# Kernel optimization log

Hardware: AMD Instinct MI355X
Metric: run time of the kernel (lower is better)

Reference implementation:

```python
import jax, jax.numpy as jnp
import numpy as np
from jax import lax

# Static problem sizes (see shape_source)
B, C, N = 32, 512, 64
SENTS_PER_VIDEO = 4
TARGETS_PER_SENT = 2
S = B * SENTS_PER_VIDEO          # 128 sentences
M = S * TARGETS_PER_SENT         # 256 target moments
P = N * (N + 1) // 2             # 2080 valid proposals (upper-tri mask2d)
T_TEMP = 0.1
MARGIN = 0.0
NEG_IOU = 0.5
K_TOP = 1                        # pos_topk
WEIGHT = 1.0


def setup_inputs() -> dict:
    key = jax.random.key(0)
    k1, k2, k3, k4 = jax.random.split(key, 4)
    return {
        "video_feats": jax.random.normal(k1, (B, C, N, N), jnp.float32),
        "sents_feats": jax.random.normal(k2, (S, C), jnp.float32),
        "num_sentences": jnp.full((B,), SENTS_PER_VIDEO, jnp.int32),
        "num_targets": jnp.full((S,), TARGETS_PER_SENT, jnp.int32),
        "iou2d": jax.random.uniform(k3, (S, N, N), jnp.float32),
        "iou2ds": jax.random.uniform(k4, (M, N, N), jnp.float32),
        "mask2d": jnp.triu(jnp.ones((N, N), bool)),
        "epoch": 0,  # < start_DNS_epoch -> DNS branch skipped
    }


def _log_cross_entropy(pos_scores, all_scores, neg_mask, t, m):
    # Faithful to LogCrossEntropy.forward
    pos_exp = jnp.exp((pos_scores - m) / t)
    neg_exp_sum = jnp.sum(jnp.exp(all_scores / t) * neg_mask, axis=-1)
    loss = -((pos_scores - m) / t - jnp.log(pos_exp + neg_exp_sum))
    return jnp.mean(loss)


def _l2_normalize(x, axis=-1, eps=1e-12):
    n = jnp.linalg.norm(x, axis=axis, keepdims=True)
    return x / jnp.maximum(n, eps)


def reference(video_feats, sents_feats, num_sentences, num_targets,
              iou2d, iou2ds, mask2d, epoch):
    # Compact valid proposals (P is static: upper-triangular mask2d)
    idx = jnp.nonzero(mask2d.reshape(-1), size=P)[0]              # (P,)
    v = video_feats.reshape(B, C, N * N)[:, :, idx]               # (B,C,P)
    v = jnp.transpose(v, (0, 2, 1))                               # (B,P,C)
    iou2d_f = iou2d.reshape(S, N * N)[:, idx]                     # (S,P)
    iou2ds_f = iou2ds.reshape(M, N * N)[:, idx]                   # (M,P)

    v = _l2_normalize(v)
    sents = _l2_normalize(sents_feats)

    scatter_s2v = jnp.repeat(jnp.arange(B), num_sentences, total_repeat_length=S)
    scatter_m2s = jnp.repeat(jnp.arange(S), num_targets, total_repeat_length=M)
    scatter_m2v = scatter_s2v[scatter_m2s]

    # top-K proposals per target moment by IoU
    topk_idx = lax.top_k(iou2ds_f, K_TOP)[1]                      # (M,K)
    topk_v = jnp.take_along_axis(v[scatter_m2v], topk_idx[:, :, None], axis=1)  # (M,K,C)

    # inter-video loss
    inter_video_pos = jnp.einsum('mkc,mc->mk', topk_v, sents[scatter_m2s])  # (M,K)
    inter_video_all = jnp.einsum('mkc,sc->mks', topk_v, sents)              # (M,K,S)
    inter_video_neg_mask = (~jnp.eye(S, dtype=bool))[scatter_m2s][:, None, :]  # (M,1,S)
    loss_inter_video = _log_cross_entropy(
        inter_video_pos, inter_video_all, inter_video_neg_mask, T_TEMP, MARGIN)

    # inter-query loss
    inter_query_pos = inter_video_pos                              # (M,K)
    inter_query_all = (sents @ v.reshape(B * P, C).T)[:, None, :]  # (S,1,B*P)
    # pos_mask: block-diagonal per video, refined by IoU > neg_iou inside own block
    onehot = jnp.eye(B, dtype=bool)[scatter_s2v]                   # (S,B)
    pos_mask = (onehot[:, :, None] & (iou2d_f > NEG_IOU)[:, None, :]).reshape(S, B * P)
    inter_query_neg_mask = (~pos_mask)[:, None, :]                 # (S,1,B*P)
    loss_inter_query = _log_cross_entropy(
        inter_query_pos, inter_query_all[scatter_m2s],
        inter_query_neg_mask[scatter_m2s], T_TEMP, MARGIN)

    total = (loss_inter_video + loss_inter_query) * WEIGHT
    return total, loss_inter_video, loss_inter_query
```

## Files before the change

kernel.cpp:

```cpp
#include <hip/hip_runtime.h>
#include <cstdint>

#define BB 32
#define CC 512
#define NSQ 4096
#define SS 128
#define MM 256
#define PP 2080
#define JJ (BB*PP)

#define WS_SN     0
#define WS_SNB    262144
#define WS_IDX    393216
#define WS_IV     401536
#define WS_NEGQ   532608

typedef short bf16x8 __attribute__((ext_vector_type(8)));
typedef float f32x4  __attribute__((ext_vector_type(4)));

__device__ __forceinline__ unsigned short f2bf(float x) {
    unsigned int u = __float_as_uint(x);
    unsigned int r = (u + 0x7fffu + ((u >> 16) & 1u)) >> 16;
    return (unsigned short)r;
}

__global__ void k_prep(const float* __restrict__ sents, float* __restrict__ sn,
                       unsigned short* __restrict__ snb,
                       int* __restrict__ idx, float* __restrict__ negq) {
    const int blk = blockIdx.x, t = threadIdx.x;
    if (blk < 128) {
        __shared__ float red[256];
        const float* row = sents + (size_t)blk * CC;
        float x0 = row[t], x1 = row[t + 256];
        red[t] = x0 * x0 + x1 * x1;
        __syncthreads();
        for (int off = 128; off > 0; off >>= 1) {
            if (t < off) red[t] += red[t + off];
            __syncthreads();
        }
        float rn = 1.0f / fmaxf(sqrtf(red[0]), 1e-12f);
        float y0 = x0 * rn, y1 = x1 * rn;
        sn[(size_t)blk * CC + t]        = y0;
        sn[(size_t)blk * CC + t + 256]  = y1;
        snb[(size_t)blk * CC + t]       = f2bf(y0);
        snb[(size_t)blk * CC + t + 256] = f2bf(y1);
    } else if (blk < 144) {
        int i = (blk - 128) * 256 + t;
        int r = i >> 6, c = i & 63;
        if (c >= r) {
            int p = r * 64 - (r * (r - 1)) / 2 + (c - r);
            idx[p] = i;
        }
    } else {
        if (t < 128) negq[t] = 0.0f;
    }
}

__global__ void k_fused(const float* __restrict__ video, const float* __restrict__ sn,
                        const float* __restrict__ iou2ds, const int* __restrict__ idx,
                        float* __restrict__ iv) {
    const int m = blockIdx.x, t = threadIdx.x;
    __shared__ float sv[256];
    __shared__ int   si[256];
    __shared__ float tvs[512];
    __shared__ float red[256];

    {
        float best = -1e30f; int bi = 1 << 30;
        const float* row = iou2ds + (size_t)m * NSQ;
        for (int p = t; p < PP; p += 256) {
            float v = row[idx[p]];
            if (v > best || (v == best && p < bi)) { best = v; bi = p; }
        }
        sv[t] = best; si[t] = bi;
        __syncthreads();
        for (int off = 128; off > 0; off >>= 1) {
            if (t < off) {
                float v2 = sv[t + off]; int i2 = si[t + off];
                if (v2 > sv[t] || (v2 == sv[t] && i2 < si[t])) { sv[t] = v2; si[t] = i2; }
            }
            __syncthreads();
        }
    }
    const int flat = idx[si[0]];
    const int b = m >> 3;

    const float* base = video + (size_t)b * CC * NSQ + flat;
    float x0 = base[(size_t)t * NSQ];
    float x1 = base[(size_t)(t + 256) * NSQ];
    red[t] = x0 * x0 + x1 * x1;
    __syncthreads();
    for (int off = 128; off > 0; off >>= 1) {
        if (t < off) red[t] += red[t + off];
        __syncthreads();
    }
    float rn = 1.0f / fmaxf(sqrtf(red[0]), 1e-12f);
    tvs[t] = x0 * rn;
    tvs[t + 256] = x1 * rn;
    __syncthreads();

    const int s = t & 127, h = t >> 7;
    const float4* a4 = (const float4*)(tvs + h * 256);
    const float4* b4 = (const float4*)(sn + (size_t)s * CC + h * 256);
    float acc = 0.f;
#pragma unroll 8
    for (int c = 0; c < 64; c++) {
        float4 a = a4[c], bb = b4[c];
        acc += a.x * bb.x + a.y * bb.y + a.z * bb.z + a.w * bb.w;
    }
    __syncthreads();
    red[t] = acc;
    __syncthreads();
    if (t < 128) iv[(size_t)m * SS + t] = red[t] + red[t + 128];
}

#define BK 64
#define LDK 72

__global__ __launch_bounds__(256)
void k_big(const float* __restrict__ video, const unsigned short* __restrict__ snb,
           const float* __restrict__ iou2d, const int* __restrict__ idx,
           float* __restrict__ negq) {
    __shared__ unsigned short sA[128 * LDK];
    __shared__ unsigned short vB[128 * LDK];
    __shared__ int   colb[128], colflat[128];
    __shared__ float colrn[128];
    __shared__ float sqpart[256];
    __shared__ float red[128][17];

    const int t    = threadIdx.x;
    const int w    = t >> 6;
    const int lane = t & 63;
    const int q    = lane >> 4;
    const int l15  = lane & 15;
    const int j0   = blockIdx.x * 128;

    if (t < 128) {
        int col = j0 + t;
        int b = col / PP;
        colb[t] = b;
        colflat[t] = idx[col - b * PP];
    }

    const int jj = t & 127;
    const int kh = t >> 7;
    int colL = j0 + jj;
    int bL = colL / PP;
    int flatL = idx[colL - bL * PP];
    const float* vbase = video + (size_t)bL * (CC * NSQ) + flatL;

    f32x4 acc[2][8];
#pragma unroll
    for (int i = 0; i < 2; i++)
#pragma unroll
        for (int j = 0; j < 8; j++) acc[i][j] = (f32x4){0.f, 0.f, 0.f, 0.f};

    float sqa = 0.f;

    for (int k0 = 0; k0 < CC; k0 += BK) {
        __syncthreads();
#pragma unroll
        for (int it = 0; it < 4; it++) {
            int lin = t + it * 256;
            int row = lin >> 3, kc = (lin & 7) * 8;
            bf16x8 v = *(const bf16x8*)(snb + (size_t)row * CC + k0 + kc);
            *(bf16x8*)(sA + row * LDK + kc) = v;
        }
        {
            const float* vp = vbase + (size_t)(k0 + kh * 32) * NSQ;
#pragma unroll
            for (int g = 0; g < 4; g++) {
                unsigned short buf[8];
#pragma unroll
                for (int i = 0; i < 8; i++) {
                    float x = vp[(size_t)(g * 8 + i) * NSQ];
                    sqa += x * x;
                    buf[i] = f2bf(x);
                }
                *(bf16x8*)(vB + jj * LDK + kh * 32 + g * 8) = *(bf16x8*)buf;
            }
        }
        __syncthreads();
#pragma unroll
        for (int ks = 0; ks < BK; ks += 32) {
            bf16x8 a[2], bfr[8];
#pragma unroll
            for (int rt = 0; rt < 2; rt++) {
                int row = w * 32 + rt * 16 + l15;
                a[rt] = *(const bf16x8*)(sA + row * LDK + ks + q * 8);
            }
#pragma unroll
            for (int ct = 0; ct < 8; ct++) {
                int col = ct * 16 + l15;
                bfr[ct] = *(const bf16x8*)(vB + col * LDK + ks + q * 8);
            }
#pragma unroll
            for (int rt = 0; rt < 2; rt++)
#pragma unroll
                for (int ct = 0; ct < 8; ct++)
                    acc[rt][ct] = __builtin_amdgcn_mfma_f32_16x16x32_bf16(
                        a[rt], bfr[ct], acc[rt][ct], 0, 0, 0);
        }
    }

    sqpart[t] = sqa;
    __syncthreads();
    if (t < 128) colrn[t] = 1.0f / fmaxf(sqrtf(sqpart[t] + sqpart[t + 128]), 1e-12f);
    __syncthreads();

#pragma unroll
    for (int rt = 0; rt < 2; rt++) {
#pragma unroll
        for (int r = 0; r < 4; r++) {
            int s = w * 32 + rt * 16 + q * 4 + r;
            float rowsum = 0.f;
#pragma unroll
            for (int ct = 0; ct < 8; ct++) {
                int c = ct * 16 + l15;
                float sc = acc[rt][ct][r] * colrn[c];
                float e = expf(sc * 10.0f);
                if ((s >> 2) == colb[c]) {
                    if (iou2d[(size_t)s * NSQ + colflat[c]] > 0.5f) e = 0.f;
                }
                rowsum += e;
            }
            red[s][l15] = rowsum;
        }
    }
    __syncthreads();
    if (t < 128) {
        float tot = 0.f;
#pragma unroll
        for (int x = 0; x < 16; x++) tot += red[t][x];
        atomicAdd(&negq[t], tot);
    }
}

__global__ void k_final(const float* __restrict__ iv, const float* __restrict__ negq,
                        float* __restrict__ out) {
    const int t = threadIdx.x;
    __shared__ float rv[256], rq[256];
    const float* row = iv + (size_t)t * SS;
    const int ms = t >> 1;
    float pos = row[ms];
    float nv = 0.f;
    for (int s = 0; s < SS; s++) {
        float e = expf(row[s] * 10.0f);
        if (s == ms) e = 0.f;
        nv += e;
    }
    float pe = expf(pos * 10.0f);
    float lv = logf(pe + nv) - pos * 10.0f;
    float lq = logf(pe + negq[ms]) - pos * 10.0f;
    rv[t] = lv; rq[t] = lq;
    __syncthreads();
    for (int off = 128; off > 0; off >>= 1) {
        if (t < off) { rv[t] += rv[t + off]; rq[t] += rq[t + off]; }
        __syncthreads();
    }
    if (t == 0) {
        float liv = rv[0] / 256.f, liq = rq[0] / 256.f;
        out[0] = liv + liq;
        out[1] = liv;
        out[2] = liq;
    }
}

extern "C" void kernel_launch(void* const* d_in, const int* in_sizes, int n_in,
                              void* d_out, int out_size, void* d_ws, size_t ws_size,
                              hipStream_t stream) {
    const float* video  = (const float*)d_in[0];
    const float* sents  = (const float*)d_in[1];
    const float* iou2d  = (const float*)d_in[4];
    const float* iou2ds = (const float*)d_in[5];
    float* out = (float*)d_out;

    char* ws = (char*)d_ws;
    float*          sn   = (float*)(ws + WS_SN);
    unsigned short* snb  = (unsigned short*)(ws + WS_SNB);
    int*            idx  = (int*)(ws + WS_IDX);
    float*          iv   = (float*)(ws + WS_IV);
    float*          negq = (float*)(ws + WS_NEGQ);

    k_prep <<<145, 256, 0, stream>>>(sents, sn, snb, idx, negq);
    k_big  <<<JJ / 128, 256, 0, stream>>>(video, snb, iou2d, idx, negq);
    k_fused<<<MM,  256, 0, stream>>>(video, sn, iou2ds, idx, iv);
    k_final<<<1,   256, 0, stream>>>(iv, negq, out);
}
```

Measured before the change: 439.0 us.

## Merge big GEMM and topk kernels into one launch with swizzled LDS

Combines k_fused and k_big into a single kernel whose first 256 blocks handle the per-target top-1 path and the remaining blocks run the bf16 MFMA similarity tile. This removes one launch and lets the two independent workloads overlap on the device. It also swaps padded LDS rows for an XOR swizzle to avoid bank conflicts, replaces the shared-memory row reduction with wave shuffles plus more atomics, uses __expf, and sets launch_bounds occupancy 4. The union-based shared memory shrinks the footprint, but register pressure may rise under the occupancy hint.

Measured after the change: 489.6 us. 1.12x slower.

```diff
diff --git a/kernel.cpp b/kernel.cpp
--- a/kernel.cpp
+++ b/kernel.cpp
@@ -8,6 +8,7 @@
 #define MM 256
 #define PP 2080
 #define JJ (BB*PP)
+#define NBIG (JJ/128)
 
 #define WS_SN     0
 #define WS_SNB    262144
@@ -56,90 +57,98 @@
     }
 }
 
-__global__ void k_fused(const float* __restrict__ video, const float* __restrict__ sn,
-                        const float* __restrict__ iou2ds, const int* __restrict__ idx,
-                        float* __restrict__ iv) {
-    const int m = blockIdx.x, t = threadIdx.x;
-    __shared__ float sv[256];
-    __shared__ int   si[256];
-    __shared__ float tvs[512];
-    __shared__ float red[256];
-
-    {
-        float best = -1e30f; int bi = 1 << 30;
-        const float* row = iou2ds + (size_t)m * NSQ;
-        for (int p = t; p < PP; p += 256) {
-            float v = row[idx[p]];
-            if (v > best || (v == best && p < bi)) { best = v; bi = p; }
-        }
-        sv[t] = best; si[t] = bi;
+
+union SMem {
+    struct {
+        unsigned short sA[128 * 64];
+        unsigned short vB[128 * 64];
+        int   colb[128];
+        int   colflat[128];
+        float colrn[128];
+        float sqpart[256];
+    } big;
+    struct {
+        float sv[256];
+        int   si[256];
+        float tvs[512];
+        float red[256];
+    } fus;
+};
+
+__global__ __launch_bounds__(256, 4)
+void k_mega(const float* __restrict__ video, const float* __restrict__ sn,
+            const unsigned short* __restrict__ snb,
+            const float* __restrict__ iou2d, const float* __restrict__ iou2ds,
+            const int* __restrict__ idx,
+            float* __restrict__ iv, float* __restrict__ negq) {
+    __shared__ SMem sm;
+    const int t = threadIdx.x;
+
+    if (blockIdx.x < MM) {
+        const int m = blockIdx.x;
+        {
+            float best = -1e30f; int bi = 1 << 30;
+            const float* row = iou2ds + (size_t)m * NSQ;
+            for (int p = t; p < PP; p += 256) {
+                float v = row[idx[p]];
+                if (v > best || (v == best && p < bi)) { best = v; bi = p; }
+            }
+            sm.fus.sv[t] = best; sm.fus.si[t] = bi;
+            __syncthreads();
+            for (int off = 128; off > 0; off >>= 1) {
+                if (t < off) {
+                    float v2 = sm.fus.sv[t + off]; int i2 = sm.fus.si[t + off];
+                    if (v2 > sm.fus.sv[t] || (v2 == sm.fus.sv[t] && i2 < sm.fus.si[t])) {
+                        sm.fus.sv[t] = v2; sm.fus.si[t] = i2;
+                    }
+                }
+                __syncthreads();
+            }
+        }
+        const int flat = idx[sm.fus.si[0]];
+        const int b = m >> 3;
+
+        const float* base = video + (size_t)b * CC * NSQ + flat;
+        float x0 = base[(size_t)t * NSQ];
+        float x1 = base[(size_t)(t + 256) * NSQ];
+        sm.fus.red[t] = x0 * x0 + x1 * x1;
         __syncthreads();
         for (int off = 128; off > 0; off >>= 1) {
-            if (t < off) {
-                float v2 = sv[t + off]; int i2 = si[t + off];
-                if (v2 > sv[t] || (v2 == sv[t] && i2 < si[t])) { sv[t] = v2; si[t] = i2; }
-            }
+            if (t < off) sm.fus.red[t] += sm.fus.red[t + off];
             __syncthreads();
         }
-    }
-    const int flat = idx[si[0]];
-    const int b = m >> 3;
-
-    const float* base = video + (size_t)b * CC * NSQ + flat;
-    float x0 = base[(size_t)t * NSQ];
-    float x1 = base[(size_t)(t + 256) * NSQ];
-    red[t] = x0 * x0 + x1 * x1;
-    __syncthreads();
-    for (int off = 128; off > 0; off >>= 1) {
-        if (t < off) red[t] += red[t + off];
-        __syncthreads();
-    }
-    float rn = 1.0f / fmaxf(sqrtf(red[0]), 1e-12f);
-    tvs[t] = x0 * rn;
-    tvs[t + 256] = x1 * rn;
-    __syncthreads();
-
-    const int s = t & 127, h = t >> 7;
-    const float4* a4 = (const float4*)(tvs + h * 256);
-    const float4* b4 = (const float4*)(sn + (size_t)s * CC + h * 256);
-    float acc = 0.f;
+        float rn = 1.0f / fmaxf(sqrtf(sm.fus.red[0]), 1e-12f);
+        sm.fus.tvs[t] = x0 * rn;
+        sm.fus.tvs[t + 256] = x1 * rn;
+        __syncthreads();
+
+        const int s = t & 127, h = t >> 7;
+        const float4* a4 = (const float4*)(sm.fus.tvs + h * 256);
+        const float4* b4 = (const float4*)(sn + (size_t)s * CC + h * 256);
+        float acc = 0.f;
 #pragma unroll 8
-    for (int c = 0; c < 64; c++) {
-        float4 a = a4[c], bb = b4[c];
-        acc += a.x * bb.x + a.y * bb.y + a.z * bb.z + a.w * bb.w;
-    }
-    __syncthreads();
-    red[t] = acc;
-    __syncthreads();
-    if (t < 128) iv[(size_t)m * SS + t] = red[t] + red[t + 128];
-}
-
-#define BK 64
-#define LDK 72
-
-__global__ __launch_bounds__(256)
-void k_big(const float* __restrict__ video, const unsigned short* __restrict__ snb,
-           const float* __restrict__ iou2d, const int* __restrict__ idx,
-           float* __restrict__ negq) {
-    __shared__ unsigned short sA[128 * LDK];
-    __shared__ unsigned short vB[128 * LDK];
-    __shared__ int   colb[128], colflat[128];
-    __shared__ float colrn[128];
-    __shared__ float sqpart[256];
-    __shared__ float red[128][17];
-
-    const int t    = threadIdx.x;
+        for (int c = 0; c < 64; c++) {
+            float4 a = a4[c], bb = b4[c];
+            acc += a.x * bb.x + a.y * bb.y + a.z * bb.z + a.w * bb.w;
+        }
+        __syncthreads();
+        sm.fus.red[t] = acc;
+        __syncthreads();
+        if (t < 128) iv[(size_t)m * SS + t] = sm.fus.red[t] + sm.fus.red[t + 128];
+        return;
+    }
+
     const int w    = t >> 6;
     const int lane = t & 63;
     const int q    = lane >> 4;
     const int l15  = lane & 15;
-    const int j0   = blockIdx.x * 128;
+    const int j0   = (blockIdx.x - MM) * 128;
 
     if (t < 128) {
         int col = j0 + t;
         int b = col / PP;
-        colb[t] = b;
-        colflat[t] = idx[col - b * PP];
+        sm.big.colb[t] = b;
+        sm.big.colflat[t] = idx[col - b * PP];
     }
 
     const int jj = t & 127;
@@ -156,15 +165,17 @@
         for (int j = 0; j < 8; j++) acc[i][j] = (f32x4){0.f, 0.f, 0.f, 0.f};
 
     float sqa = 0.f;
-
-    for (int k0 = 0; k0 < CC; k0 += BK) {
+    const int swzA_w = jj & 7;
+    (void)swzA_w;
+
+    for (int k0 = 0; k0 < CC; k0 += 64) {
         __syncthreads();
 #pragma unroll
         for (int it = 0; it < 4; it++) {
             int lin = t + it * 256;
-            int row = lin >> 3, kc = (lin & 7) * 8;
-            bf16x8 v = *(const bf16x8*)(snb + (size_t)row * CC + k0 + kc);
-            *(bf16x8*)(sA + row * LDK + kc) = v;
+            int row = lin >> 3, G = lin & 7;
+            bf16x8 v = *(const bf16x8*)(snb + (size_t)row * CC + k0 + G * 8);
+            *(bf16x8*)(sm.big.sA + row * 64 + ((G ^ (row & 7)) * 8)) = v;
         }
         {
             const float* vp = vbase + (size_t)(k0 + kh * 32) * NSQ;
@@ -177,22 +188,24 @@
                     sqa += x * x;
                     buf[i] = f2bf(x);
                 }
-                *(bf16x8*)(vB + jj * LDK + kh * 32 + g * 8) = *(bf16x8*)buf;
-            }
-        }
-        __syncthreads();
-#pragma unroll
-        for (int ks = 0; ks < BK; ks += 32) {
+                int G = kh * 4 + g;
+                *(bf16x8*)(sm.big.vB + jj * 64 + ((G ^ (jj & 7)) * 8)) = *(bf16x8*)buf;
+            }
+        }
+        __syncthreads();
+#pragma unroll
+        for (int ks = 0; ks < 64; ks += 32) {
+            const int so = ((q + (ks >> 3)) ^ (l15 & 7)) * 8;
             bf16x8 a[2], bfr[8];
 #pragma unroll
             for (int rt = 0; rt < 2; rt++) {
                 int row = w * 32 + rt * 16 + l15;
-                a[rt] = *(const bf16x8*)(sA + row * LDK + ks + q * 8);
+                a[rt] = *(const bf16x8*)(sm.big.sA + row * 64 + so);
             }
 #pragma unroll
             for (int ct = 0; ct < 8; ct++) {
                 int col = ct * 16 + l15;
-                bfr[ct] = *(const bf16x8*)(vB + col * LDK + ks + q * 8);
+                bfr[ct] = *(const bf16x8*)(sm.big.vB + col * 64 + so);
             }
 #pragma unroll
             for (int rt = 0; rt < 2; rt++)
@@ -203,9 +216,10 @@
         }
     }
 
-    sqpart[t] = sqa;
+    sm.big.sqpart[t] = sqa;
     __syncthreads();
-    if (t < 128) colrn[t] = 1.0f / fmaxf(sqrtf(sqpart[t] + sqpart[t + 128]), 1e-12f);
+    if (t < 128)
+        sm.big.colrn[t] = 1.0f / fmaxf(sqrtf(sm.big.sqpart[t] + sm.big.sqpart[t + 128]), 1e-12f);
     __syncthreads();
 
 #pragma unroll
@@ -217,22 +231,18 @@
 #pragma unroll
             for (int ct = 0; ct < 8; ct++) {
                 int c = ct * 16 + l15;
-                float sc = acc[rt][ct][r] * colrn[c];
-                float e = expf(sc * 10.0f);
-                if ((s >> 2) == colb[c]) {
-                    if (iou2d[(size_t)s * NSQ + colflat[c]] > 0.5f) e = 0.f;
+                float sc = acc[rt][ct][r] * sm.big.colrn[c];
+                float e = __expf(sc * 10.0f);
+                if ((s >> 2) == sm.big.colb[c]) {
+                    if (iou2d[(size_t)s * NSQ + sm.big.colflat[c]] > 0.5f) e = 0.f;
                 }
                 rowsum += e;
             }
-            red[s][l15] = rowsum;
-        }
-    }
-    __syncthreads();
-    if (t < 128) {
-        float tot = 0.f;
-#pragma unroll
-        for (int x = 0; x < 16; x++) tot += red[t][x];
-        atomicAdd(&negq[t], tot);
+#pragma unroll
+            for (int msk = 1; msk < 16; msk <<= 1)
+                rowsum += __shfl_xor(rowsum, msk, 64);
+            if (l15 == 0) atomicAdd(&negq[s], rowsum);
+        }
     }
 }
 
@@ -283,7 +293,6 @@
     float*          negq = (float*)(ws + WS_NEGQ);
 
     k_prep <<<145, 256, 0, stream>>>(sents, sn, snb, idx, negq);
-    k_big  <<<JJ / 128, 256, 0, stream>>>(video, snb, iou2d, idx, negq);
-    k_fused<<<MM,  256, 0, stream>>>(video, sn, iou2ds, idx, iv);
-    k_final<<<1,   256, 0, stream>>>(iv, negq, out);
-}
+    k_mega <<<MM + NBIG, 256, 0, stream>>>(video, sn, snb, iou2d, iou2ds, idx, iv, negq);
+    k_final<<<1, 256, 0, stream>>>(iv, negq, out);
+}
```
